# Performance work log

Measured on AMD Instinct MI355X. Metric: run time of the kernel, lower is better.

Reference implementation:

```python
import jax, jax.numpy as jnp
import numpy as np


def setup_inputs() -> dict:
    key = jax.random.key(0)
    x = jax.random.normal(key, (16, 512, 512, 8), dtype=jnp.float32)
    # 3x3 structuring element with center False: neighbors-only local max
    mask = jnp.array([[True, True, True],
                      [True, False, True],
                      [True, True, True]])
    return {"x": x, "mask": mask}


def reference(x, mask):
    # Equivalent of tf.nn.dilation2d(x, where(mask, 0, -inf), SAME, stride 1):
    # masked_max[b,i,j,c] = max over (di,dj) in mask of x[b,i+di-ph, j+dj-pw, c]
    # (out-of-bounds treated as -inf, matching dilation's identity padding).
    kh, kw = mask.shape  # small static window (e.g. 3x3)
    H, W = x.shape[1], x.shape[2]
    ph, pw = (kh - 1) // 2, (kw - 1) // 2
    neg_inf = jnp.asarray(-jnp.inf, x.dtype)
    xp = jnp.pad(x, ((0, 0), (ph, kh - 1 - ph), (pw, kw - 1 - pw), (0, 0)),
                 constant_values=-np.inf)
    masked_max = jnp.full_like(x, -np.inf)
    for di in range(kh):          # fixed small kernel loop (9 taps), not a data-dim loop
        for dj in range(kw):
            win = xp[:, di:di + H, dj:dj + W, :]
            masked_max = jnp.maximum(masked_max, jnp.where(mask[di, dj], win, neg_inf))
    # suppressed = cast(x > masked_max) * x
    return (x > masked_max).astype(x.dtype) * x
```

## Files before the change

### kernel.cpp

```cpp
#include <hip/hip_runtime.h>
#include <math.h>


constexpr int Hdim = 512;
constexpr int Wdim = 512;
constexpr int HPT  = 8;
constexpr int ROWS = HPT + 2;
constexpr int ROW  = Wdim * 2;

__device__ __forceinline__ float4 f4max(float4 a, float4 b) {
    return make_float4(fmaxf(a.x,b.x), fmaxf(a.y,b.y), fmaxf(a.z,b.z), fmaxf(a.w,b.w));
}

__global__ __launch_bounds__(256) void nms_kernel(
    const float4* __restrict__ x,
    const unsigned char* __restrict__ mask_bytes,
    float4* __restrict__ out)
{
    const int* mi = (const int*)mask_bytes;
    bool intlay = true;
    #pragma unroll
    for (int i = 0; i < 9; ++i) { int v = mi[i]; intlay = intlay && (v == 0 || v == 1); }
    bool m[9];
    #pragma unroll
    for (int i = 0; i < 9; ++i) m[i] = intlay ? (mi[i] != 0) : (mask_bytes[i] != 0);

    int gid = blockIdx.x * blockDim.x + threadIdx.x;
    int c4 = gid & 1;
    int w  = (gid >> 1) & (Wdim - 1);
    int hg = (gid >> 10) & 63;
    int n  = gid >> 16;
    int h0 = hg * HPT;

    const float4 NEG = make_float4(-INFINITY, -INFINITY, -INFINITY, -INFINITY);
    bool aok = (w > 0), cok = (w < Wdim - 1);
    int ao = aok ? -2 : 0;
    int co = cok ?  2 : 0;

    int base = ((n * Hdim + h0) * Wdim + w) * 2 + c4;

    float4 A[ROWS], B[ROWS], C[ROWS];
    #pragma unroll
    for (int r = 0; r < ROWS; ++r) {
        int hr = h0 - 1 + r;
        int hc = hr < 0 ? 0 : (hr > Hdim - 1 ? Hdim - 1 : hr);
        int rb = base + (hc - h0) * ROW;
        A[r] = x[rb + ao];
        B[r] = x[rb];
        C[r] = x[rb + co];
    }

    bool topclamp = (h0 == 0);
    bool botclamp = (h0 + HPT == Hdim);

    #pragma unroll
    for (int s = 0; s < HPT; ++s) {
        bool r0ok = !(s == 0 && topclamp);
        bool r2ok = !(s == HPT - 1 && botclamp);

        float4 va = NEG, vb = NEG, vc = NEG;
        if (m[0] && r0ok) va = f4max(va, A[s]);
        if (m[3])         va = f4max(va, A[s + 1]);
        if (m[6] && r2ok) va = f4max(va, A[s + 2]);
        if (m[1] && r0ok) vb = f4max(vb, B[s]);
        if (m[4])         vb = f4max(vb, B[s + 1]);
        if (m[7] && r2ok) vb = f4max(vb, B[s + 2]);
        if (m[2] && r0ok) vc = f4max(vc, C[s]);
        if (m[5])         vc = f4max(vc, C[s + 1]);
        if (m[8] && r2ok) vc = f4max(vc, C[s + 2]);

        va.x = aok ? va.x : -INFINITY; va.y = aok ? va.y : -INFINITY;
        va.z = aok ? va.z : -INFINITY; va.w = aok ? va.w : -INFINITY;
        vc.x = cok ? vc.x : -INFINITY; vc.y = cok ? vc.y : -INFINITY;
        vc.z = cok ? vc.z : -INFINITY; vc.w = cok ? vc.w : -INFINITY;

        float4 mm = f4max(f4max(va, vb), vc);
        float4 ctr = B[s + 1];
        float4 o;
        o.x = (ctr.x > mm.x) ? ctr.x : 0.0f;
        o.y = (ctr.y > mm.y) ? ctr.y : 0.0f;
        o.z = (ctr.z > mm.z) ? ctr.z : 0.0f;
        o.w = (ctr.w > mm.w) ? ctr.w : 0.0f;
        out[base + s * ROW] = o;
    }
}

extern "C" void kernel_launch(void* const* d_in, const int* in_sizes, int n_in,
                              void* d_out, int out_size, void* d_ws, size_t ws_size,
                              hipStream_t stream) {
    const float4* x = (const float4*)d_in[0];
    const unsigned char* mask = (const unsigned char*)d_in[1];
    float4* out = (float4*)d_out;

    int total = 16 * (Hdim / HPT) * Wdim * 2;
    int block = 256;
    int grid = total / block;
    nms_kernel<<<grid, block, 0, stream>>>(x, mask, out);
}
```

Baseline: 230.2 us.

## Stream rows through a rolling register window and raise occupancy hint

Replaces the kernel that loads all 10 rows x 3 columns into register arrays with a rolling scheme. It prefetches the next row while computing per-row partial maxima, keeping only a few carried registers. It also sets launch_bounds min blocks per CU to 8, cutting register pressure for higher occupancy in a memory-bound stencil. The trade-off is less memory-level parallelism per thread, since fewer loads are in flight at once, and a possible register cap causing spills.

```diff
diff --git a/kernel.cpp b/kernel.cpp
--- a/kernel.cpp
+++ b/kernel.cpp
@@ -12,7 +12,7 @@
     return make_float4(fmaxf(a.x,b.x), fmaxf(a.y,b.y), fmaxf(a.z,b.z), fmaxf(a.w,b.w));
 }
 
-__global__ __launch_bounds__(256) void nms_kernel(
+__global__ __launch_bounds__(256, 8) void nms_kernel(
     const float4* __restrict__ x,
     const unsigned char* __restrict__ mask_bytes,
     float4* __restrict__ out)
@@ -36,52 +36,66 @@
     bool aok = (w > 0), cok = (w < Wdim - 1);
     int ao = aok ? -2 : 0;
     int co = cok ?  2 : 0;
+    bool topclamp = (h0 == 0);
+    bool botclamp = (h0 + HPT == Hdim);
 
     int base = ((n * Hdim + h0) * Wdim + w) * 2 + c4;
 
-    float4 A[ROWS], B[ROWS], C[ROWS];
+    auto rowoff = [&](int r) -> int {
+        int roff = (r - 1) * ROW;
+        if (r == 0 && topclamp) roff = 0;
+        if (r == ROWS - 1 && botclamp) roff = (HPT - 1) * ROW;
+        return roff;
+    };
+
+    float4 A, Bv, C, pA, pB, pC;
+    {
+        int rb = base + rowoff(0);
+        A = x[rb + ao]; Bv = x[rb]; C = x[rb + co];
+    }
+
+    float4 R0p2 = NEG, R0p1 = NEG, R1p1 = NEG, CTp1 = NEG;
+
     #pragma unroll
     for (int r = 0; r < ROWS; ++r) {
-        int hr = h0 - 1 + r;
-        int hc = hr < 0 ? 0 : (hr > Hdim - 1 ? Hdim - 1 : hr);
-        int rb = base + (hc - h0) * ROW;
-        A[r] = x[rb + ao];
-        B[r] = x[rb];
-        C[r] = x[rb + co];
-    }
+        if (r < ROWS - 1) {
+            int rb = base + rowoff(r + 1);
+            pA = x[rb + ao]; pB = x[rb]; pC = x[rb + co];
+        }
 
-    bool topclamp = (h0 == 0);
-    bool botclamp = (h0 + HPT == Hdim);
+        float4 a = A, b = Bv, c = C;
+        a.x = aok ? a.x : -INFINITY; a.y = aok ? a.y : -INFINITY;
+        a.z = aok ? a.z : -INFINITY; a.w = aok ? a.w : -INFINITY;
+        c.x = cok ? c.x : -INFINITY; c.y = cok ? c.y : -INFINITY;
+        c.z = cok ? c.z : -INFINITY; c.w = cok ? c.w : -INFINITY;
 
-    #pragma unroll
-    for (int s = 0; s < HPT; ++s) {
-        bool r0ok = !(s == 0 && topclamp);
-        bool r2ok = !(s == HPT - 1 && botclamp);
+        float4 R0 = NEG, R1 = NEG, R2 = NEG;
+        if (m[0]) R0 = f4max(R0, a);
+        if (m[1]) R0 = f4max(R0, b);
+        if (m[2]) R0 = f4max(R0, c);
+        if (m[3]) R1 = f4max(R1, a);
+        if (m[4]) R1 = f4max(R1, b);
+        if (m[5]) R1 = f4max(R1, c);
+        if (m[6]) R2 = f4max(R2, a);
+        if (m[7]) R2 = f4max(R2, b);
+        if (m[8]) R2 = f4max(R2, c);
+        if (r == 0 && topclamp)        R0 = NEG;
+        if (r == ROWS - 1 && botclamp) R2 = NEG;
 
-        float4 va = NEG, vb = NEG, vc = NEG;
-        if (m[0] && r0ok) va = f4max(va, A[s]);
-        if (m[3])         va = f4max(va, A[s + 1]);
-        if (m[6] && r2ok) va = f4max(va, A[s + 2]);
-        if (m[1] && r0ok) vb = f4max(vb, B[s]);
-        if (m[4])         vb = f4max(vb, B[s + 1]);
-        if (m[7] && r2ok) vb = f4max(vb, B[s + 2]);
-        if (m[2] && r0ok) vc = f4max(vc, C[s]);
-        if (m[5])         vc = f4max(vc, C[s + 1]);
-        if (m[8] && r2ok) vc = f4max(vc, C[s + 2]);
+        if (r >= 2) {
+            int s = r - 2;
+            float4 mm = f4max(f4max(R0p2, R1p1), R2);
+            float4 ctr = CTp1;
+            float4 o;
+            o.x = (ctr.x > mm.x) ? ctr.x : 0.0f;
+            o.y = (ctr.y > mm.y) ? ctr.y : 0.0f;
+            o.z = (ctr.z > mm.z) ? ctr.z : 0.0f;
+            o.w = (ctr.w > mm.w) ? ctr.w : 0.0f;
+            out[base + s * ROW] = o;
+        }
 
-        va.x = aok ? va.x : -INFINITY; va.y = aok ? va.y : -INFINITY;
-        va.z = aok ? va.z : -INFINITY; va.w = aok ? va.w : -INFINITY;
-        vc.x = cok ? vc.x : -INFINITY; vc.y = cok ? vc.y : -INFINITY;
-        vc.z = cok ? vc.z : -INFINITY; vc.w = cok ? vc.w : -INFINITY;
-
-        float4 mm = f4max(f4max(va, vb), vc);
-        float4 ctr = B[s + 1];
-        float4 o;
-        o.x = (ctr.x > mm.x) ? ctr.x : 0.0f;
-        o.y = (ctr.y > mm.y) ? ctr.y : 0.0f;
-        o.z = (ctr.z > mm.z) ? ctr.z : 0.0f;
-        o.w = (ctr.w > mm.w) ? ctr.w : 0.0f;
-        out[base + s * ROW] = o;
+        R0p2 = R0p1; R0p1 = R0; R1p1 = R1; CTp1 = Bv;
+        A = pA; Bv = pB; C = pC;
     }
 }
 
```

Measured after the change: 238.6 us. 3.6% more time.

## Stage 2D halo tiles in shared memory and compute separable row maxima

Applied to the files above, without the earlier changes.

Each block now loads an 8x64-pixel tile plus a one-pixel halo into LDS with padded -inf borders, replacing the per-thread redundant global loads of left/center/right columns over 10 rows. Threads then read neighbours from LDS and keep a rolling window of per-row partial maxima, so each loaded row is reused across three output rows. This cuts global read amplification (roughly 3x plus vertical halo) at the cost of LDS traffic, a block barrier and extra halo loads. Launch bounds also request higher occupancy.

```diff
diff --git a/kernel.cpp b/kernel.cpp
--- a/kernel.cpp
+++ b/kernel.cpp
@@ -4,19 +4,23 @@
 
 constexpr int Hdim = 512;
 constexpr int Wdim = 512;
-constexpr int HPT  = 8;
-constexpr int ROWS = HPT + 2;
 constexpr int ROW  = Wdim * 2;
+constexpr int TH   = 8;
+constexpr int TW   = 64;
+constexpr int LROWS = TH + 2;
+constexpr int LCOLS = TW * 2 + 4;
 
 __device__ __forceinline__ float4 f4max(float4 a, float4 b) {
     return make_float4(fmaxf(a.x,b.x), fmaxf(a.y,b.y), fmaxf(a.z,b.z), fmaxf(a.w,b.w));
 }
 
-__global__ __launch_bounds__(256) void nms_kernel(
+__global__ __launch_bounds__(256, 7) void nms_kernel(
     const float4* __restrict__ x,
     const unsigned char* __restrict__ mask_bytes,
     float4* __restrict__ out)
 {
+    __shared__ float4 lds[LROWS][LCOLS];
+
     const int* mi = (const int*)mask_bytes;
     bool intlay = true;
     #pragma unroll
@@ -25,63 +29,77 @@
     #pragma unroll
     for (int i = 0; i < 9; ++i) m[i] = intlay ? (mi[i] != 0) : (mask_bytes[i] != 0);
 
-    int gid = blockIdx.x * blockDim.x + threadIdx.x;
-    int c4 = gid & 1;
-    int w  = (gid >> 1) & (Wdim - 1);
-    int hg = (gid >> 10) & 63;
-    int n  = gid >> 16;
-    int h0 = hg * HPT;
+    const float4 NEG = make_float4(-INFINITY, -INFINITY, -INFINITY, -INFINITY);
 
-    const float4 NEG = make_float4(-INFINITY, -INFINITY, -INFINITY, -INFINITY);
-    bool aok = (w > 0), cok = (w < Wdim - 1);
-    int ao = aok ? -2 : 0;
-    int co = cok ?  2 : 0;
+    int b  = blockIdx.x;
+    int wg = b & 7;
+    int hg = (b >> 3) & 63;
+    int n  = b >> 9;
+    int h0 = hg * TH;
+    int w0 = wg * TW;
+    int t  = threadIdx.x;
 
-    int base = ((n * Hdim + h0) * Wdim + w) * 2 + c4;
+    int gb = ((n * Hdim + (h0 - 1)) * Wdim + w0) * 2;
+    #pragma unroll
+    for (int i = 0; i < 5; ++i) {
+        int idx = t + i * 256;
+        int r = idx >> 7;
+        int c = idx & 127;
+        int h = h0 - 1 + r;
+        float4 v = NEG;
+        if (h >= 0 && h < Hdim)
+            v = x[gb + r * ROW + c];
+        lds[r][2 + c] = v;
+    }
+    if (t < 40) {
+        int r    = t >> 2;
+        int q    = t & 3;
+        int side = q >> 1;
+        int c4   = q & 1;
+        int h    = h0 - 1 + r;
+        int wgl  = side ? (w0 + TW) : (w0 - 1);
+        float4 v = NEG;
+        if (h >= 0 && h < Hdim && wgl >= 0 && wgl < Wdim)
+            v = x[((n * Hdim + h) * Wdim + wgl) * 2 + c4];
+        lds[r][side ? (2 + 2 * TW + c4) : c4] = v;
+    }
+    __syncthreads();
 
-    float4 A[ROWS], B[ROWS], C[ROWS];
+    int cidx = t & 127;
+    int hb   = (t >> 7) * 4;
+    int col  = 2 + cidx;
+    int obase = ((n * Hdim + h0) * Wdim + w0) * 2 + cidx;
+
+    float4 R0a = NEG, R0b = NEG, R1b = NEG, CTb = NEG;
     #pragma unroll
-    for (int r = 0; r < ROWS; ++r) {
-        int hr = h0 - 1 + r;
-        int hc = hr < 0 ? 0 : (hr > Hdim - 1 ? Hdim - 1 : hr);
-        int rb = base + (hc - h0) * ROW;
-        A[r] = x[rb + ao];
-        B[r] = x[rb];
-        C[r] = x[rb + co];
-    }
+    for (int k = 0; k < 6; ++k) {
+        int r = hb + k;
+        float4 a  = lds[r][col - 2];
+        float4 bb = lds[r][col];
+        float4 cc = lds[r][col + 2];
 
-    bool topclamp = (h0 == 0);
-    bool botclamp = (h0 + HPT == Hdim);
+        float4 R0 = NEG, R1 = NEG, R2 = NEG;
+        if (m[0]) R0 = f4max(R0, a);
+        if (m[1]) R0 = f4max(R0, bb);
+        if (m[2]) R0 = f4max(R0, cc);
+        if (m[3]) R1 = f4max(R1, a);
+        if (m[4]) R1 = f4max(R1, bb);
+        if (m[5]) R1 = f4max(R1, cc);
+        if (m[6]) R2 = f4max(R2, a);
+        if (m[7]) R2 = f4max(R2, bb);
+        if (m[8]) R2 = f4max(R2, cc);
 
-    #pragma unroll
-    for (int s = 0; s < HPT; ++s) {
-        bool r0ok = !(s == 0 && topclamp);
-        bool r2ok = !(s == HPT - 1 && botclamp);
-
-        float4 va = NEG, vb = NEG, vc = NEG;
-        if (m[0] && r0ok) va = f4max(va, A[s]);
-        if (m[3])         va = f4max(va, A[s + 1]);
-        if (m[6] && r2ok) va = f4max(va, A[s + 2]);
-        if (m[1] && r0ok) vb = f4max(vb, B[s]);
-        if (m[4])         vb = f4max(vb, B[s + 1]);
-        if (m[7] && r2ok) vb = f4max(vb, B[s + 2]);
-        if (m[2] && r0ok) vc = f4max(vc, C[s]);
-        if (m[5])         vc = f4max(vc, C[s + 1]);
-        if (m[8] && r2ok) vc = f4max(vc, C[s + 2]);
-
-        va.x = aok ? va.x : -INFINITY; va.y = aok ? va.y : -INFINITY;
-        va.z = aok ? va.z : -INFINITY; va.w = aok ? va.w : -INFINITY;
-        vc.x = cok ? vc.x : -INFINITY; vc.y = cok ? vc.y : -INFINITY;
-        vc.z = cok ? vc.z : -INFINITY; vc.w = cok ? vc.w : -INFINITY;
-
-        float4 mm = f4max(f4max(va, vb), vc);
-        float4 ctr = B[s + 1];
-        float4 o;
-        o.x = (ctr.x > mm.x) ? ctr.x : 0.0f;
-        o.y = (ctr.y > mm.y) ? ctr.y : 0.0f;
-        o.z = (ctr.z > mm.z) ? ctr.z : 0.0f;
-        o.w = (ctr.w > mm.w) ? ctr.w : 0.0f;
-        out[base + s * ROW] = o;
+        if (k >= 2) {
+            float4 mm  = f4max(f4max(R0a, R1b), R2);
+            float4 ctr = CTb;
+            float4 o;
+            o.x = (ctr.x > mm.x) ? ctr.x : 0.0f;
+            o.y = (ctr.y > mm.y) ? ctr.y : 0.0f;
+            o.z = (ctr.z > mm.z) ? ctr.z : 0.0f;
+            o.w = (ctr.w > mm.w) ? ctr.w : 0.0f;
+            out[obase + (hb + k - 2) * ROW] = o;
+        }
+        R0a = R0b; R0b = R0; R1b = R1; CTb = bb;
     }
 }
 
@@ -92,8 +110,7 @@
     const unsigned char* mask = (const unsigned char*)d_in[1];
     float4* out = (float4*)d_out;
 
-    int total = 16 * (Hdim / HPT) * Wdim * 2;
+    int grid = 16 * (Hdim / TH) * (Wdim / TW);
     int block = 256;
-    int grid = total / block;
     nms_kernel<<<grid, block, 0, stream>>>(x, mask, out);
 }
```

Measured after the change: 241.3 us. 4.8% more time.
